# Performance work log

Hardware: AMD Instinct MI355X
Metric: run time of the kernel (lower is better)

Reference implementation:

```python
import math
import jax, jax.numpy as jnp
import numpy as np

# ---- constants (module-level in the original source) ----
_CMAG_A = 0.75
_CMAG_B = 120.0
_CMAG_K = 17.3
_DEG2RAD = math.pi / 180.0
AMP = 100.0
_SPREAD = math.sqrt(AMP / 675.0)
VIEW_ANGLE = 90.0
MAP_SIZE = 256
SOFT_MATCH_SIGMA = 1.5
RENDER_CHUNK = 50
N_SHANK = 10            # N_CONTACTPOINTS_SHANK -> 10^3 = 1000 contacts
SPACING = 0.4           # SPACING_ALONG_XY (mm)


def setup_inputs() -> dict:
    key = jax.random.key(0)
    ks = jax.random.split(key, 12)
    B, V, N = 8, 10000, N_SHANK ** 3
    # bounded params: alpha, beta, offset, shank_length
    alpha = jax.random.uniform(ks[0], (B,), minval=-60.0, maxval=60.0)
    beta = jax.random.uniform(ks[1], (B,), minval=0.0, maxval=90.0)
    offset = jax.random.uniform(ks[2], (B,), minval=0.0, maxval=3.0)
    shank = jax.random.uniform(ks[3], (B,), minval=8.0, maxval=12.0)
    params = jnp.stack([alpha, beta, offset, shank], axis=-1).astype(jnp.float32)
    electrode_logits = jax.random.normal(ks[4], (B, N), dtype=jnp.float32)
    start_loc = jnp.array([30.0, -40.0, 10.0], dtype=jnp.float32)
    # V1 voxel positions clustered around the insertion start point
    v1_pos = start_loc + jax.random.uniform(ks[5], (V, 3), minval=-25.0, maxval=25.0)
    pol = jax.random.uniform(ks[6], (V,), minval=0.0, maxval=360.0)
    ecc = jax.random.uniform(ks[7], (V,), minval=0.2, maxval=12.0)
    sig = jax.random.uniform(ks[8], (V,), minval=0.5, maxval=3.0)
    v1_prf = jnp.stack([pol, ecc, sig], axis=-1).astype(jnp.float32)
    surf_dist_lut = jax.random.uniform(ks[9], (37, 26), minval=10.0, maxval=20.0)
    alpha_grid = jnp.linspace(-90.0, 90.0, 37, dtype=jnp.float32)
    beta_grid = jnp.linspace(-15.0, 110.0, 26, dtype=jnp.float32)
    # contact grid template [n^3, 3] = (x, y, z_frac)
    yv = jnp.arange(N_SHANK, dtype=jnp.float32) * SPACING
    xv = jnp.arange(N_SHANK, dtype=jnp.float32) * SPACING
    zf = jnp.linspace(0.0, 1.0, N_SHANK, dtype=jnp.float32)
    yy, xx, zz = jnp.meshgrid(yv, xv, zf, indexing='ij')
    grid_template = jnp.stack([xx, yy, zz], axis=-1).reshape(-1, 3)
    return {
        'params': params,
        'electrode_logits': electrode_logits,
        'v1_pos': v1_pos.astype(jnp.float32),
        'v1_prf': v1_prf,
        'start_loc': start_loc,
        'surf_dist_lut': surf_dist_lut.astype(jnp.float32),
        'alpha_grid': alpha_grid,
        'beta_grid': beta_grid,
        'grid_template': grid_template,
    }


def _rotation_matrix(alpha_deg, beta_deg):
    a = alpha_deg * _DEG2RAD
    b = beta_deg * _DEG2RAD
    ca, sa = jnp.cos(a), jnp.sin(a)
    cb, sb = jnp.cos(b), jnp.sin(b)
    ones = jnp.ones_like(a)
    zeros = jnp.zeros_like(a)
    Rx = jnp.stack([jnp.stack([ones, zeros, zeros], -1),
                    jnp.stack([zeros, ca, -sa], -1),
                    jnp.stack([zeros, sa, ca], -1)], axis=-2)
    Ry = jnp.stack([jnp.stack([cb, zeros, sb], -1),
                    jnp.stack([zeros, ones, zeros], -1),
                    jnp.stack([-sb, zeros, cb], -1)], axis=-2)
    return Rx @ Ry  # [B,3,3]


def _interp_surface_dist(alpha, beta, lut, a_grid, b_grid):
    # bilinear grid_sample with align_corners=True + border padding == clamped
    # pixel-space bilinear interpolation
    na, nb = lut.shape
    a_norm = 2.0 * (alpha - a_grid[0]) / (a_grid[-1] - a_grid[0] + 1e-08) - 1.0
    b_norm = 2.0 * (beta - b_grid[0]) / (b_grid[-1] - b_grid[0] + 1e-08) - 1.0
    ai = jnp.clip((a_norm + 1.0) * 0.5 * (na - 1), 0.0, na - 1.0)
    bi = jnp.clip((b_norm + 1.0) * 0.5 * (nb - 1), 0.0, nb - 1.0)
    a0 = jnp.clip(jnp.floor(ai), 0, na - 1).astype(jnp.int32)
    b0 = jnp.clip(jnp.floor(bi), 0, nb - 1).astype(jnp.int32)
    a1 = jnp.minimum(a0 + 1, na - 1)
    b1 = jnp.minimum(b0 + 1, nb - 1)
    fa = ai - a0.astype(ai.dtype)
    fb = bi - b0.astype(bi.dtype)
    v00 = lut[a0, b0]; v01 = lut[a0, b1]; v10 = lut[a1, b0]; v11 = lut[a1, b1]
    out = (v00 * (1 - fa) * (1 - fb) + v01 * (1 - fa) * fb
           + v10 * fa * (1 - fb) + v11 * fa * fb)
    return jnp.maximum(out, 1.0)


def _forward(params, electrode_logits, v1_pos, v1_prf, start_loc,
             surf_dist_lut, alpha_grid, beta_grid, grid_template):
    B = params.shape[0]
    N = grid_template.shape[0]
    H = W = MAP_SIZE
    alpha, beta, offset, shank = (params[:, 0], params[:, 1], params[:, 2], params[:, 3])
    elec_prob = jax.nn.sigmoid(electrode_logits)

    # ---- positioned contact grid [B,N,3] ----
    xy = jnp.broadcast_to(grid_template[None, :, :2], (B, N, 2))
    z = grid_template[None, :, 2:3] * shank[:, None, None]
    grid = jnp.concatenate([xy, z], axis=-1)
    grid = grid - grid.mean(axis=1, keepdims=True)
    R = _rotation_matrix(alpha, beta)
    rotated = jnp.einsum('bnc,bdc->bnd', grid, R)   # grid @ R^T
    ref = jnp.array([0.0, 0.0, -1.0], dtype=params.dtype)
    direction = jnp.einsum('bij,j->bi', R, ref)
    direction = direction / jnp.linalg.norm(direction, axis=-1, keepdims=True)
    surf_dist = _interp_surface_dist(alpha, beta, surf_dist_lut, alpha_grid, beta_grid)
    penetration = surf_dist - shank / 2.0 - offset
    grid_center = start_loc[None, :] + direction * penetration[:, None]
    contact_pos = rotated + grid_center[:, None, :]

    # ---- soft PRF lookup via gaussian kernel matching (avoid [B,N,V,3] diff) ----
    p2 = jnp.sum(contact_pos ** 2, axis=-1)          # [B,N]
    v2 = jnp.sum(v1_pos ** 2, axis=-1)               # [V]
    cross = jnp.einsum('bnc,vc->bnv', contact_pos, v1_pos)
    d2 = jnp.maximum(p2[:, :, None] + v2[None, None, :] - 2.0 * cross, 0.0)
    weights = jnp.exp(-d2 / (2.0 * SOFT_MATCH_SIGMA ** 2))   # [B,N,V]
    wsum = weights.sum(axis=-1)
    validity = jnp.minimum(wsum, 1.0)
    weights_norm = weights / (wsum[:, :, None] + 1e-08)
    prf = jnp.einsum('bnv,vp->bnp', weights_norm, v1_prf)    # [B,N,3]

    # ---- chunked gaussian splatting -> [B,1,H,W] ----
    angle_rad = prf[:, :, 0] * _DEG2RAD
    ecc = prf[:, :, 1]
    m = _CMAG_K * (1.0 / (ecc + _CMAG_A) - 1.0 / (ecc + _CMAG_B))
    m_inv = 1.0 / (jnp.abs(m) + 1e-08)
    phos_sigma = _SPREAD * m_inv / 2.0
    scaled_ecc = H / VIEW_ANGLE
    cx = ecc * jnp.cos(angle_rad) * scaled_ecc + H / 2.0
    cy = ecc * jnp.sin(angle_rad) * scaled_ecc + W / 2.0
    phos_size = jnp.maximum(phos_sigma * scaled_ecc, 1.0)
    w = elec_prob * validity

    gy, gx = jnp.meshgrid(jnp.arange(H, dtype=params.dtype),
                          jnp.arange(W, dtype=params.dtype), indexing='ij')
    n_chunks = N // RENDER_CHUNK
    def to_chunks(t):  # [B,N] -> [n_chunks,B,chunk]
        return t.reshape(B, n_chunks, RENDER_CHUNK).transpose(1, 0, 2)
    scan_in = (to_chunks(cx), to_chunks(cy), to_chunks(phos_size), to_chunks(w))

    def body(acc, ch):
        cx_, cy_, s_, w_ = ch  # [B,chunk]
        g = jnp.exp(-((gx[None, None] - cx_[:, :, None, None]) ** 2
                      + (gy[None, None] - cy_[:, :, None, None]) ** 2)
                    / (s_[:, :, None, None] ** 2 + 1e-08))
        return acc + jnp.einsum('bchw,bc->bhw', g, w_), None

    phos_map, _ = jax.lax.scan(body, jnp.zeros((B, H, W), dtype=params.dtype), scan_in)
    phos_map = jnp.rot90(phos_map, k=1, axes=(-2, -1))
    max_val = phos_map.reshape(B, -1).max(axis=1)[:, None, None]
    phos_map = phos_map / (max_val + 1e-08)
    return phos_map[:, None, :, :]


def reference(params, electrode_logits, v1_pos, v1_prf, start_loc,
              surf_dist_lut, alpha_grid, beta_grid, grid_template):
    return _forward(params, electrode_logits, v1_pos, v1_prf, start_loc,
                    surf_dist_lut, alpha_grid, beta_grid, grid_template)
```

## Files before the change

kernel.cpp:

```cpp
#include <hip/hip_runtime.h>
#include <math.h>

#define WS_MAP    0
#define WS_CNT    524416
#define WS_EPOS   524736
#define WS_CPOS   557504
#define WS_CPRF   885184
#define WS_PART   1049024
#define WS_MAX    2359744

#define NB 8
#define NN 1000
#define NV 10000
#define NSEG 40
#define SEGCAP 256
#define NEB 1024

__global__ __launch_bounds__(256) void k_cull(const float* __restrict__ params,
                                              const float* __restrict__ start_loc,
                                              const float* __restrict__ lut,
                                              const float* __restrict__ agrid,
                                              const float* __restrict__ bgrid,
                                              const float* __restrict__ v1_pos,
                                              const float* __restrict__ v1_prf,
                                              const float* __restrict__ tmpl,
                                              float* __restrict__ ws) {
    __shared__ float sst[NB*16];
    __shared__ int   lcnt[NB];
    int g = blockIdx.x, t = threadIdx.x;
    int v = g*256 + t;
    float4* mp = (float4*)(ws + WS_MAP);
    #pragma unroll
    for (int k = 0; k < 13; ++k) {
        int idx = k*10240 + v;
        if (idx < 131072) mp[idx] = make_float4(0.f,0.f,0.f,0.f);
    }
    if (g == 0 && t < NB) ws[WS_MAX + t] = 0.f;
    if (t < NB) lcnt[t] = 0;
    if (t < NB) {
        int b = t;
        float alpha = params[b*4+0], beta = params[b*4+1];
        float off   = params[b*4+2], shank = params[b*4+3];
        const float D2R = 0.017453292519943295f;
        float a = alpha*D2R, bb = beta*D2R;
        float ca = cosf(a), sa = sinf(a), cb = cosf(bb), sb = sinf(bb);
        float r00=cb,     r01=0.f, r02=sb;
        float r10=sa*sb,  r11=ca,  r12=-sa*cb;
        float r20=-ca*sb, r21=sa,  r22=ca*cb;
        float dx=-r02, dy=-r12, dz=-r22;
        float inv = rsqrtf(dx*dx+dy*dy+dz*dz);
        dx*=inv; dy*=inv; dz*=inv;
        float ag0=agrid[0], agN=agrid[36], bg0=bgrid[0], bgN=bgrid[25];
        float an = 2.f*(alpha-ag0)/(agN-ag0+1e-8f) - 1.f;
        float bn = 2.f*(beta -bg0)/(bgN-bg0+1e-8f) - 1.f;
        float ai = fminf(fmaxf((an+1.f)*0.5f*36.f, 0.f), 36.f);
        float bi = fminf(fmaxf((bn+1.f)*0.5f*25.f, 0.f), 25.f);
        int a0 = (int)floorf(ai); a0 = a0<0?0:(a0>36?36:a0);
        int b0 = (int)floorf(bi); b0 = b0<0?0:(b0>25?25:b0);
        int a1 = a0+1>36?36:a0+1;
        int b1 = b0+1>25?25:b0+1;
        float fa = ai - (float)a0, fb = bi - (float)b0;
        float v00=lut[a0*26+b0], v01=lut[a0*26+b1], v10=lut[a1*26+b0], v11=lut[a1*26+b1];
        float sd = v00*(1.f-fa)*(1.f-fb) + v01*(1.f-fa)*fb + v10*fa*(1.f-fb) + v11*fa*fb;
        sd = fmaxf(sd, 1.f);
        float pen = sd - shank*0.5f - off;
        float hs = shank*0.5f;
        sst[b*16+0]=r00; sst[b*16+1]=r01; sst[b*16+2]=r02;
        sst[b*16+3]=r10; sst[b*16+4]=r11; sst[b*16+5]=r12;
        sst[b*16+6]=r20; sst[b*16+7]=r21; sst[b*16+8]=r22;
        sst[b*16+9]  = start_loc[0] + dx*pen;
        sst[b*16+10] = start_loc[1] + dy*pen;
        sst[b*16+11] = start_loc[2] + dz*pen;
        sst[b*16+12] = shank;
        sst[b*16+13] = fabsf(r00)*1.8f + fabsf(r01)*1.8f + fabsf(r02)*hs;
        sst[b*16+14] = fabsf(r10)*1.8f + fabsf(r11)*1.8f + fabsf(r12)*hs;
        sst[b*16+15] = fabsf(r20)*1.8f + fabsf(r21)*1.8f + fabsf(r22)*hs;
    }
    __syncthreads();
    const float C = -0.32059889797532524f;
    if (v < 8192) {
        float4* ep = (float4*)(ws + WS_EPOS);
        if (v < NB*NN) {
            int b = v/1000, n = v - b*1000;
            const float* st = sst + b*16;
            float gx = tmpl[n*3]-1.8f, gy = tmpl[n*3+1]-1.8f;
            float gz = (tmpl[n*3+2]-0.5f)*st[12];
            float px = st[0]*gx + st[1]*gy + st[2]*gz + st[9];
            float py = st[3]*gx + st[4]*gy + st[5]*gz + st[10];
            float pz = st[6]*gx + st[7]*gy + st[8]*gz + st[11];
            ep[v] = make_float4(px, py, pz, C*(px*px+py*py+pz*pz));
        } else {
            ep[v] = make_float4(0.f, 0.f, 0.f, -1e30f);
        }
    }
    bool valid = v < NV;
    float x=0.f, y=0.f, z=0.f, pol=0.f, ecc=0.f;
    if (valid) {
        x = v1_pos[v*3]; y = v1_pos[v*3+1]; z = v1_pos[v*3+2];
        pol = v1_prf[v*3]; ecc = v1_prf[v*3+1];
    }
    float4 payload = make_float4(-2.f*C*x, -2.f*C*y, -2.f*C*z, C*(x*x+y*y+z*z));
    int lane = t & 63;
    float4* cpos = (float4*)(ws + WS_CPOS);
    float2* cprf = (float2*)(ws + WS_CPRF);
    #pragma unroll
    for (int b = 0; b < NB; ++b) {
        const float* st = sst + b*16;
        float dxc = fmaxf(fabsf(x - st[9])  - st[13], 0.f);
        float dyc = fmaxf(fabsf(y - st[10]) - st[14], 0.f);
        float dzc = fmaxf(fabsf(z - st[11]) - st[15], 0.f);
        bool pred = valid && (dxc*dxc + dyc*dyc + dzc*dzc <= 90.f);
        unsigned long long m = __ballot(pred);
        int base = 0;
        if (lane == 0) base = atomicAdd(&lcnt[b], (int)__popcll(m));
        base = __shfl(base, 0, 64);
        if (pred) {
            int my = base + (int)__popcll(m & ((1ull << lane) - 1ull));
            int slot = b*10240 + g*SEGCAP + my;
            cpos[slot] = payload;
            cprf[slot] = make_float2(pol, ecc);
        }
    }
    __syncthreads();
    if (t < NB) ((int*)(ws + WS_CNT))[g*NB + t] = lcnt[t];
}

__global__ __launch_bounds__(256) void k_match(float* __restrict__ ws) {
    __shared__ float4 sq[SEGCAP];
    __shared__ float2 spe[SEGCAP];
    int g = blockIdx.x, t = threadIdx.x;
    int b = g / 80, r = g - b*80, q = r >> 1, eg = r & 1;
    int cq = ((const int*)(ws + WS_CNT))[q*NB + b];
    if (t < cq) {
        sq[t]  = ((const float4*)(ws + WS_CPOS))[b*10240 + q*SEGCAP + t];
        spe[t] = ((const float2*)(ws + WS_CPRF))[b*10240 + q*SEGCAP + t];
    }
    __syncthreads();
    const float4* ep = (const float4*)(ws + WS_EPOS);
    int n0 = eg*512 + t, n1 = n0 + 256;
    float4 P0 = (n0 < NN) ? ep[b*NN + n0] : make_float4(0.f,0.f,0.f,-1e30f);
    float4 P1 = (n1 < NN) ? ep[b*NN + n1] : make_float4(0.f,0.f,0.f,-1e30f);
    float sw0=0.f,sp0=0.f,se0=0.f, sw1=0.f,sp1=0.f,se1=0.f;
    #pragma unroll 2
    for (int i = 0; i < cq; ++i) {
        float4 qq = sq[i];
        float2 pe = spe[i];
        float a0 = fmaf(qq.x, P0.x, fmaf(qq.y, P0.y, fmaf(qq.z, P0.z, P0.w + qq.w)));
        float w0 = __builtin_amdgcn_exp2f(a0);
        sw0 += w0; sp0 = fmaf(w0, pe.x, sp0); se0 = fmaf(w0, pe.y, se0);
        float a1 = fmaf(qq.x, P1.x, fmaf(qq.y, P1.y, fmaf(qq.z, P1.z, P1.w + qq.w)));
        float w1 = __builtin_amdgcn_exp2f(a1);
        sw1 += w1; sp1 = fmaf(w1, pe.x, sp1); se1 = fmaf(w1, pe.y, se1);
    }
    float4* part = (float4*)(ws + WS_PART);
    int baseq = (b*NSEG + q)*NEB;
    part[baseq + n0] = make_float4(sw0, sp0, se0, 0.f);
    part[baseq + n1] = make_float4(sw1, sp1, se1, 0.f);
}

__global__ __launch_bounds__(256) void k_prender(const float* __restrict__ logits,
                                                 float* __restrict__ ws) {
    __shared__ float4 red[4][64];
    __shared__ float4 par[64];
    int g = blockIdx.x, t = threadIdx.x, lane = t & 63, w = t >> 6;
    int b = g >> 4, E0 = (g & 15) * 64;
    const float4* part = (const float4*)(ws + WS_PART);
    int el = E0 + lane;
    float sw = 0.f, sp = 0.f, se = 0.f;
    #pragma unroll
    for (int i = 0; i < 10; ++i) {
        float4 p = part[(b*NSEG + (w + i*4))*NEB + el];
        sw += p.x; sp += p.y; se += p.z;
    }
    red[w][lane] = make_float4(sw, sp, se, 0.f);
    __syncthreads();
    if (w == 0) {
        float4 a = red[0][lane], b4 = red[1][lane], c4 = red[2][lane], d4 = red[3][lane];
        sw = (a.x+b4.x) + (c4.x+d4.x);
        sp = (a.y+b4.y) + (c4.y+d4.y);
        se = (a.z+b4.z) + (c4.z+d4.z);
        float denom = sw + 1e-8f;
        float pol = sp/denom, eccv = se/denom;
        float validity = fminf(sw, 1.f);
        int n = E0 + lane;
        float lg = (n < NN) ? logits[b*NN + n] : 0.f;
        float prob = 1.f/(1.f + __expf(-lg));
        float wgt = (n < NN) ? prob * validity : 0.f;
        float ang = pol * 0.017453292519943295f;
        float m1 = 17.3f*(1.f/(eccv+0.75f) - 1.f/(eccv+120.f));
        float minv = 1.f/(fabsf(m1)+1e-8f);
        float sig  = 0.3849001794597506f * minv * 0.5f;
        const float scl = 256.f/90.f;
        float s = fmaxf(sig*scl, 1.f);
        float invden = 1.f/(s*s + 1e-8f);
        par[lane] = make_float4(eccv*__cosf(ang)*scl + 128.f,
                                eccv*__sinf(ang)*scl + 128.f, invden, wgt);
    }
    __syncthreads();
    int ix = lane & 7, iy = lane >> 3;
    for (int k = 0; k < 16; ++k) {
        int el2 = k*4 + w;
        float4 P = par[el2];
        if (P.w <= 0.f) continue;
        int fx = (int)floorf(P.x), fy = (int)floorf(P.y);
        int X = fx - 3 + ix, Y = fy - 3 + iy;
        if (X >= 0 && X < 256 && Y >= 0 && Y < 256) {
            float dx = (float)X - P.x, dy = (float)Y - P.y;
            float d2 = dx*dx + dy*dy;
            if (d2 <= 12.25f)
                atomicAdd(ws + WS_MAP + b*65536 + Y*256 + X, P.w * __expf(-d2 * P.z));
        }
    }
}

__global__ __launch_bounds__(256) void k_max(float* __restrict__ ws) {
    int g = blockIdx.x;
    int b = g >> 4;
    const float4* m = (const float4*)(ws + WS_MAP + b*65536 + (g & 15)*4096);
    float mx = 0.f;
    #pragma unroll
    for (int k = 0; k < 4; ++k) {
        float4 v = m[k*256 + threadIdx.x];
        mx = fmaxf(mx, fmaxf(fmaxf(v.x, v.y), fmaxf(v.z, v.w)));
    }
    #pragma unroll
    for (int s2 = 32; s2 >= 1; s2 >>= 1) mx = fmaxf(mx, __shfl_xor(mx, s2, 64));
    __shared__ float red[4];
    if ((threadIdx.x & 63) == 0) red[threadIdx.x >> 6] = mx;
    __syncthreads();
    if (threadIdx.x == 0) {
        mx = fmaxf(fmaxf(red[0], red[1]), fmaxf(red[2], red[3]));
        atomicMax((unsigned int*)(ws + WS_MAX + b), __float_as_uint(mx));
    }
}

__global__ __launch_bounds__(256) void k_final(const float* __restrict__ ws,
                                               float* __restrict__ out) {
    __shared__ float tile[32][33];
    int g  = blockIdx.x;
    int b  = g >> 6;
    int t6 = g & 63;
    int r0 = (t6 >> 3) * 32;
    int c0 = (t6 & 7) * 32;
    int ic0 = 224 - r0;
    int j  = threadIdx.x & 31;
    int i0 = threadIdx.x >> 5;
    const float* m = ws + WS_MAP + b*65536;
    #pragma unroll
    for (int p = 0; p < 4; ++p) {
        int i = i0 + p*8;
        tile[i][j] = m[(c0+i)*256 + ic0 + j];
    }
    __syncthreads();
    float inv = 1.f/(ws[WS_MAX + b] + 1e-8f);
    #pragma unroll
    for (int p = 0; p < 4; ++p) {
        int k = i0 + p*8;
        out[b*65536 + (r0+k)*256 + c0 + j] = tile[j][31-k] * inv;
    }
}

extern "C" void kernel_launch(void* const* d_in, const int* in_sizes, int n_in,
                              void* d_out, int out_size, void* d_ws, size_t ws_size,
                              hipStream_t stream) {
    const float* params    = (const float*)d_in[0];
    const float* logits    = (const float*)d_in[1];
    const float* v1_pos    = (const float*)d_in[2];
    const float* v1_prf    = (const float*)d_in[3];
    const float* start_loc = (const float*)d_in[4];
    const float* lut       = (const float*)d_in[5];
    const float* agrid     = (const float*)d_in[6];
    const float* bgrid     = (const float*)d_in[7];
    const float* tmpl      = (const float*)d_in[8];
    float* ws  = (float*)d_ws;
    float* out = (float*)d_out;

    k_cull   <<<40,  256, 0, stream>>>(params, start_loc, lut, agrid, bgrid,
                                       v1_pos, v1_prf, tmpl, ws);
    k_match  <<<640, 256, 0, stream>>>(ws);
    k_prender<<<128, 256, 0, stream>>>(logits, ws);
    k_max    <<<128, 256, 0, stream>>>(ws);
    k_final  <<<512, 256, 0, stream>>>(ws, out);
}
```

Baseline: 102.8 us.

## Fuse map max into splat render and merge segment pairs in match

The separate max-reduction kernel is removed. Its work is folded into the render kernel, which takes the running maximum of the values returned by the atomicAdd on each pixel and then reduces that per block into one atomicMax per batch. Separately, each k_match block now loads two culled voxel segments into shared memory instead of one. That halves the block count and the number of partial-sum slabs k_prender has to read. The cost is one fewer launch and fewer partial reads, in exchange for longer per-block loops and lower parallelism in k_match (320 blocks on a large GPU).

```diff
diff --git a/kernel.cpp b/kernel.cpp
--- a/kernel.cpp
+++ b/kernel.cpp
@@ -7,12 +7,13 @@
 #define WS_CPOS   557504
 #define WS_CPRF   885184
 #define WS_PART   1049024
-#define WS_MAX    2359744
+#define WS_MAX    1704384
 
 #define NB 8
 #define NN 1000
 #define NV 10000
 #define NSEG 40
+#define NSEG2 20
 #define SEGCAP 256
 #define NEB 1024
 
@@ -126,16 +127,25 @@
 }
 
 __global__ __launch_bounds__(256) void k_match(float* __restrict__ ws) {
-    __shared__ float4 sq[SEGCAP];
-    __shared__ float2 spe[SEGCAP];
+    __shared__ float4 sq[2*SEGCAP];
+    __shared__ float2 spe[2*SEGCAP];
     int g = blockIdx.x, t = threadIdx.x;
-    int b = g / 80, r = g - b*80, q = r >> 1, eg = r & 1;
-    int cq = ((const int*)(ws + WS_CNT))[q*NB + b];
-    if (t < cq) {
-        sq[t]  = ((const float4*)(ws + WS_CPOS))[b*10240 + q*SEGCAP + t];
-        spe[t] = ((const float2*)(ws + WS_CPRF))[b*10240 + q*SEGCAP + t];
-    }
-    __syncthreads();
+    int b = g / 40, r = g - b*40, qp = r >> 1, eg = r & 1;
+    int q0 = qp*2, q1 = qp*2 + 1;
+    const int* cnt = (const int*)(ws + WS_CNT);
+    int c0 = cnt[q0*NB + b], c1 = cnt[q1*NB + b];
+    const float4* cpos = (const float4*)(ws + WS_CPOS);
+    const float2* cprf = (const float2*)(ws + WS_CPRF);
+    if (t < c0) {
+        sq[t]  = cpos[b*10240 + q0*SEGCAP + t];
+        spe[t] = cprf[b*10240 + q0*SEGCAP + t];
+    }
+    if (t < c1) {
+        sq[c0 + t]  = cpos[b*10240 + q1*SEGCAP + t];
+        spe[c0 + t] = cprf[b*10240 + q1*SEGCAP + t];
+    }
+    __syncthreads();
+    int cq = c0 + c1;
     const float4* ep = (const float4*)(ws + WS_EPOS);
     int n0 = eg*512 + t, n1 = n0 + 256;
     float4 P0 = (n0 < NN) ? ep[b*NN + n0] : make_float4(0.f,0.f,0.f,-1e30f);
@@ -153,7 +163,7 @@
         sw1 += w1; sp1 = fmaf(w1, pe.x, sp1); se1 = fmaf(w1, pe.y, se1);
     }
     float4* part = (float4*)(ws + WS_PART);
-    int baseq = (b*NSEG + q)*NEB;
+    int baseq = (b*NSEG2 + qp)*NEB;
     part[baseq + n0] = make_float4(sw0, sp0, se0, 0.f);
     part[baseq + n1] = make_float4(sw1, sp1, se1, 0.f);
 }
@@ -162,14 +172,15 @@
                                                  float* __restrict__ ws) {
     __shared__ float4 red[4][64];
     __shared__ float4 par[64];
+    __shared__ float  mred[4];
     int g = blockIdx.x, t = threadIdx.x, lane = t & 63, w = t >> 6;
     int b = g >> 4, E0 = (g & 15) * 64;
     const float4* part = (const float4*)(ws + WS_PART);
     int el = E0 + lane;
     float sw = 0.f, sp = 0.f, se = 0.f;
     #pragma unroll
-    for (int i = 0; i < 10; ++i) {
-        float4 p = part[(b*NSEG + (w + i*4))*NEB + el];
+    for (int i = 0; i < 5; ++i) {
+        float4 p = part[(b*NSEG2 + (w + i*4))*NEB + el];
         sw += p.x; sp += p.y; se += p.z;
     }
     red[w][lane] = make_float4(sw, sp, se, 0.f);
@@ -198,6 +209,7 @@
     }
     __syncthreads();
     int ix = lane & 7, iy = lane >> 3;
+    float mx = 0.f;
     for (int k = 0; k < 16; ++k) {
         int el2 = k*4 + w;
         float4 P = par[el2];
@@ -207,29 +219,19 @@
         if (X >= 0 && X < 256 && Y >= 0 && Y < 256) {
             float dx = (float)X - P.x, dy = (float)Y - P.y;
             float d2 = dx*dx + dy*dy;
-            if (d2 <= 12.25f)
-                atomicAdd(ws + WS_MAP + b*65536 + Y*256 + X, P.w * __expf(-d2 * P.z));
+            if (d2 <= 12.25f) {
+                float val = P.w * __expf(-d2 * P.z);
+                float old = atomicAdd(ws + WS_MAP + b*65536 + Y*256 + X, val);
+                mx = fmaxf(mx, old + val);
+            }
         }
     }
-}
-
-__global__ __launch_bounds__(256) void k_max(float* __restrict__ ws) {
-    int g = blockIdx.x;
-    int b = g >> 4;
-    const float4* m = (const float4*)(ws + WS_MAP + b*65536 + (g & 15)*4096);
-    float mx = 0.f;
-    #pragma unroll
-    for (int k = 0; k < 4; ++k) {
-        float4 v = m[k*256 + threadIdx.x];
-        mx = fmaxf(mx, fmaxf(fmaxf(v.x, v.y), fmaxf(v.z, v.w)));
-    }
     #pragma unroll
     for (int s2 = 32; s2 >= 1; s2 >>= 1) mx = fmaxf(mx, __shfl_xor(mx, s2, 64));
-    __shared__ float red[4];
-    if ((threadIdx.x & 63) == 0) red[threadIdx.x >> 6] = mx;
-    __syncthreads();
-    if (threadIdx.x == 0) {
-        mx = fmaxf(fmaxf(red[0], red[1]), fmaxf(red[2], red[3]));
+    if (lane == 0) mred[w] = mx;
+    __syncthreads();
+    if (t == 0) {
+        mx = fmaxf(fmaxf(mred[0], mred[1]), fmaxf(mred[2], mred[3]));
         atomicMax((unsigned int*)(ws + WS_MAX + b), __float_as_uint(mx));
     }
 }
@@ -277,8 +279,7 @@
 
     k_cull   <<<40,  256, 0, stream>>>(params, start_loc, lut, agrid, bgrid,
                                        v1_pos, v1_prf, tmpl, ws);
-    k_match  <<<640, 256, 0, stream>>>(ws);
+    k_match  <<<320, 256, 0, stream>>>(ws);
     k_prender<<<128, 256, 0, stream>>>(logits, ws);
-    k_max    <<<128, 256, 0, stream>>>(ws);
     k_final  <<<512, 256, 0, stream>>>(ws, out);
 }
```

New measurement: 101.7 us. Within noise of the previous version (-1.2%).
